# Performance work log

Hardware: AMD Instinct MI355X
Metric: run time of the kernel (lower is better)

The kernel has to match this reference:

```python
import jax, jax.numpy as jnp
import numpy as np

N_NODES = 50000
N_EDGES = 600000
D = 128
NUM_GRAPHS = 64


def gcn_conv(x, W, b, edge_index, edge_weight, n):
    """PyG GCNConv: y = D^-1/2 (A+I) D^-1/2 (x W) + b, with self-loop weight 1."""
    h = x @ W  # [n, out]
    src, dst = edge_index[0], edge_index[1]
    if edge_weight is None:
        edge_weight = jnp.ones(src.shape, dtype=x.dtype)
    # append self loops
    loop = jnp.arange(n)
    src_f = jnp.concatenate([src, loop])
    dst_f = jnp.concatenate([dst, loop])
    w_f = jnp.concatenate([edge_weight, jnp.ones((n,), dtype=x.dtype)])
    deg = jax.ops.segment_sum(w_f, dst_f, num_segments=n)
    dis = jnp.where(deg > 0, jax.lax.rsqrt(jnp.maximum(deg, 1e-12)), 0.0)
    norm = dis[src_f] * w_f * dis[dst_f]  # [E+n]
    msg = h[src_f] * norm[:, None]
    out = jax.ops.segment_sum(msg, dst_f, num_segments=n)
    return out + b


def setup_inputs() -> dict:
    key = jax.random.key(0)
    ks = jax.random.split(key, 24)
    def w(k, shape, scale=0.05):
        return jax.random.normal(k, shape, dtype=jnp.float32) * scale
    inp = {
        'x': jax.random.normal(ks[0], (N_NODES, D), dtype=jnp.float32),
        'edge_index': jax.random.randint(ks[1], (2, N_EDGES), 0, N_NODES),
        'edge_attr': jax.random.uniform(ks[2], (N_EDGES, 4), dtype=jnp.float32),
        'batch': jnp.sort(jax.random.randint(ks[3], (N_NODES,), 0, NUM_GRAPHS)),
        'W1A': w(ks[4], (D, D)), 'b1A': jnp.zeros((D,), jnp.float32),
        'W1B': w(ks[5], (D, D)), 'b1B': jnp.zeros((D,), jnp.float32),
        'W1C': w(ks[6], (D, D)), 'b1C': jnp.zeros((D,), jnp.float32),
        'W1D': w(ks[7], (D, D)), 'b1D': jnp.zeros((D,), jnp.float32),
        'W2': w(ks[8], (4 * D, 2 * D)), 'b2': jnp.zeros((2 * D,), jnp.float32),
        'W3': w(ks[9], (2 * D, D)), 'b3': jnp.zeros((D,), jnp.float32),
        'Wm1': w(ks[10], (2 * D, 8)), 'bm1': jnp.zeros((8,), jnp.float32),
        'Wm2': w(ks[11], (8, 2)), 'bm2': jnp.zeros((2,), jnp.float32),
    }
    return inp


def reference(x, edge_index, edge_attr, batch, W1A, b1A, W1B, b1B, W1C, b1C,
              W1D, b1D, W2, b2, W3, b3, Wm1, bm1, Wm2, bm2):
    n = x.shape[0]
    xA = jax.nn.relu(gcn_conv(x, W1A, b1A, edge_index, edge_attr[:, 0], n))
    xB = jax.nn.relu(gcn_conv(x, W1B, b1B, edge_index, edge_attr[:, 1], n))
    xC = jax.nn.relu(gcn_conv(x, W1C, b1C, edge_index, edge_attr[:, 2], n))
    xD = jax.nn.relu(gcn_conv(x, W1D, b1D, edge_index, edge_attr[:, 3], n))
    h = jnp.concatenate([xA, xB, xC, xD], axis=1)  # [n, 4D]
    h = jax.nn.relu(gcn_conv(h, W2, b2, edge_index, None, n))
    h = gcn_conv(h, W3, b3, edge_index, None, n)  # [n, D]
    # global mean / max pool over graphs
    counts = jax.ops.segment_sum(jnp.ones((n,), h.dtype), batch, num_segments=NUM_GRAPHS)
    sums = jax.ops.segment_sum(h, batch, num_segments=NUM_GRAPHS)
    mean = sums / jnp.maximum(counts, 1.0)[:, None]
    mx = jax.ops.segment_max(h, batch, num_segments=NUM_GRAPHS)
    mx = jnp.where(counts[:, None] > 0, mx, 0.0)
    g = jnp.concatenate([mean, mx], axis=1)  # [G, 2D]
    # dropout is identity in eval mode
    logits = jax.nn.relu(g @ Wm1 + bm1) @ Wm2 + bm2
    return logits
```

## Files before the change

kernel.cpp:

```cpp
#include <hip/hip_runtime.h>

#define DEV_INLINE __device__ __forceinline__

typedef __attribute__((ext_vector_type(8))) short bf16x8;
typedef __attribute__((ext_vector_type(4))) float floatx4;

DEV_INLINE unsigned fencode(float f) {
  unsigned u = __float_as_uint(f);
  return (u & 0x80000000u) ? ~u : (u | 0x80000000u);
}
DEV_INLINE float fdecode(unsigned k) {
  return __uint_as_float((k & 0x80000000u) ? (k ^ 0x80000000u) : ~k);
}

DEV_INLINE unsigned short bf16_rne(float x) {
  unsigned u = __float_as_uint(x);
  unsigned r = (u + 0x7FFFu + ((u >> 16) & 1u)) >> 16;
  return (unsigned short)r;
}
DEV_INLINE float bf2f(unsigned short u) {
  return __uint_as_float(((unsigned)u) << 16);
}

#pragma clang diagnostic ignored "-Waddress-space-conversion"
DEV_INLINE void gload_lds16(const void* g, void* l) {
  __builtin_amdgcn_global_load_lds(
      (const __attribute__((address_space(1))) unsigned int*)g,
      (__attribute__((address_space(3))) unsigned int*)l, 16, 0, 0);
}

__global__ __launch_bounds__(256)
void prep_kernel(const float* __restrict__ WA, const float* __restrict__ WB,
                 const float* __restrict__ WC, const float* __restrict__ WD,
                 const float* __restrict__ bA, const float* __restrict__ bB,
                 const float* __restrict__ bC, const float* __restrict__ bD,
                 const float* __restrict__ W2, const float* __restrict__ W3,
                 unsigned short* __restrict__ W1t, unsigned short* __restrict__ W2t,
                 unsigned short* __restrict__ W3t, float* __restrict__ biascat) {
  int i = blockIdx.x * 256 + threadIdx.x;
  if (i < 65536) {
    int z = i >> 14, rem = i & 16383, j = rem >> 7, k = rem & 127;
    const float* W = (z == 0) ? WA : (z == 1) ? WB : (z == 2) ? WC : WD;
    W1t[i] = bf16_rne(W[k * 128 + j]);
  } else if (i < 196608) {
    int i2 = i - 65536, j = i2 >> 9, k = i2 & 511;
    W2t[i2] = bf16_rne(W2[k * 256 + j]);
  } else if (i < 229376) {
    int i3 = i - 196608, j = i3 >> 8, k = i3 & 255;
    W3t[i3] = bf16_rne(W3[k * 128 + j]);
  } else if (i < 229888) {
    int i4 = i - 229376, c = i4 >> 7, j = i4 & 127;
    const float* b = (c == 0) ? bA : (c == 1) ? bB : (c == 2) ? bC : bD;
    biascat[i4] = b[j];
  }
}

__global__ __launch_bounds__(256)
void xcast_kernel(const float* __restrict__ x, unsigned short* __restrict__ xb, int total4) {
  int i = blockIdx.x * 256 + threadIdx.x;
  if (i >= total4) return;
  float4 v = ((const float4*)x)[i];
  ushort4 o;
  o.x = bf16_rne(v.x); o.y = bf16_rne(v.y); o.z = bf16_rne(v.z); o.w = bf16_rne(v.w);
  ((ushort4*)xb)[i] = o;
}

__global__ __launch_bounds__(256)
void hist_kernel(const int* __restrict__ ei, int* __restrict__ cnt, int E) {
  int e = blockIdx.x * 256 + threadIdx.x;
  if (e < E) atomicAdd(&cnt[ei[E + e]], 1);
}

__global__ __launch_bounds__(256)
void scan1_kernel(const int* __restrict__ cnt, int* __restrict__ local,
                  int* __restrict__ bsum, int n) {
  __shared__ int s[256];
  int tid = threadIdx.x;
  int i = blockIdx.x * 256 + tid;
  int v = (i < n) ? cnt[i] : 0;
  s[tid] = v;
  __syncthreads();
#pragma unroll
  for (int off = 1; off < 256; off <<= 1) {
    int t = (tid >= off) ? s[tid - off] : 0;
    __syncthreads();
    s[tid] += t;
    __syncthreads();
  }
  if (i < n) local[i] = s[tid] - v;
  if (tid == 255) bsum[blockIdx.x] = s[255];
}

__global__ __launch_bounds__(256)
void scan2_kernel(int* __restrict__ bsum, int nb) {
  __shared__ int s[256];
  int tid = threadIdx.x;
  int v = (tid < nb) ? bsum[tid] : 0;
  s[tid] = v;
  __syncthreads();
#pragma unroll
  for (int off = 1; off < 256; off <<= 1) {
    int t = (tid >= off) ? s[tid - off] : 0;
    __syncthreads();
    s[tid] += t;
    __syncthreads();
  }
  if (tid < nb) bsum[tid] = s[tid] - v;
}

__global__ __launch_bounds__(256)
void scan3_kernel(const int* __restrict__ local, const int* __restrict__ bsum,
                  int* __restrict__ rowptr, int* __restrict__ rowwork, int n, int E) {
  int i = blockIdx.x * 256 + threadIdx.x;
  if (i < n) {
    int rp = local[i] + bsum[blockIdx.x];
    rowptr[i] = rp;
    rowwork[i] = rp;
  }
  if (i == 0) rowptr[n] = E;
}

__global__ __launch_bounds__(256)
void fill_kernel(const int* __restrict__ ei, int* __restrict__ rowwork,
                 int* __restrict__ csr, int* __restrict__ csr_src,
                 int* __restrict__ csr_dst, int E) {
  int e = blockIdx.x * 256 + threadIdx.x;
  if (e >= E) return;
  int d = ei[E + e];
  int pos = atomicAdd(&rowwork[d], 1);
  csr[pos] = e;
  csr_src[pos] = ei[e];
  csr_dst[pos] = d;
}

__global__ __launch_bounds__(256)
void degcsr_kernel(const int* __restrict__ rowptr, const int* __restrict__ csr,
                   const float* __restrict__ eattr, float* __restrict__ dis, int n) {
  int d = blockIdx.x * 256 + threadIdx.x;
  if (d >= n) return;
  int beg = rowptr[d], end = rowptr[d + 1];
  float s0 = 1.f, s1 = 1.f, s2 = 1.f, s3 = 1.f;
  for (int i = beg; i < end; ++i) {
    int e = csr[i];
    float4 w = ((const float4*)eattr)[e];
    s0 += w.x; s1 += w.y; s2 += w.z; s3 += w.w;
  }
  dis[d]         = 1.0f / sqrtf(s0);
  dis[n + d]     = 1.0f / sqrtf(s1);
  dis[2 * n + d] = 1.0f / sqrtf(s2);
  dis[3 * n + d] = 1.0f / sqrtf(s3);
  dis[4 * n + d] = 1.0f / sqrtf(1.0f + (float)(end - beg));
}

__global__ __launch_bounds__(256)
void edgeprep_kernel(const int* __restrict__ csr, const int* __restrict__ csr_src,
                     const int* __restrict__ csr_dst, const float* __restrict__ eattr,
                     const float* __restrict__ dis, float4* __restrict__ norm4,
                     float* __restrict__ norm1, int n, int E) {
  int i = blockIdx.x * 256 + threadIdx.x;
  if (i >= E) return;
  int e = csr[i], s = csr_src[i], d = csr_dst[i];
  float4 w = ((const float4*)eattr)[e];
  float4 o;
  o.x = dis[s] * w.x * dis[d];
  o.y = dis[n + s] * w.y * dis[n + d];
  o.z = dis[2 * n + s] * w.z * dis[2 * n + d];
  o.w = dis[3 * n + s] * w.w * dis[3 * n + d];
  norm4[i] = o;
  norm1[i] = dis[4 * n + s] * dis[4 * n + d];
}

__global__ __launch_bounds__(256)
void agg4x_kernel(const unsigned short* __restrict__ xb,
                  unsigned short* __restrict__ xa,
                  const int* __restrict__ rowptr, const int* __restrict__ csr_src,
                  const float4* __restrict__ norm4, const float* __restrict__ dis,
                  int n, int npad) {
  int d = blockIdx.x * 4 + (threadIdx.x >> 6);
  if (d >= n) return;
  int t = threadIdx.x & 63;
  float dc0 = dis[d], dc1 = dis[n + d], dc2 = dis[2 * n + d], dc3 = dis[3 * n + d];
  const ushort2* x2 = (const ushort2*)xb;
  ushort2 xu = x2[(size_t)d * 64 + t];
  float xvx = bf2f(xu.x), xvy = bf2f(xu.y);
  float a0x = xvx * dc0 * dc0, a0y = xvy * dc0 * dc0;
  float a1x = xvx * dc1 * dc1, a1y = xvy * dc1 * dc1;
  float a2x = xvx * dc2 * dc2, a2y = xvy * dc2 * dc2;
  float a3x = xvx * dc3 * dc3, a3y = xvy * dc3 * dc3;
  int beg = rowptr[d], end = rowptr[d + 1];
  int i = beg;
  for (; i + 4 <= end; i += 4) {
    int s0 = csr_src[i], s1 = csr_src[i + 1], s2 = csr_src[i + 2], s3 = csr_src[i + 3];
    float4 m0 = norm4[i], m1 = norm4[i + 1], m2 = norm4[i + 2], m3 = norm4[i + 3];
    ushort2 u0 = x2[(size_t)s0 * 64 + t];
    ushort2 u1 = x2[(size_t)s1 * 64 + t];
    ushort2 u2 = x2[(size_t)s2 * 64 + t];
    ushort2 u3 = x2[(size_t)s3 * 64 + t];
    float h0x = bf2f(u0.x), h0y = bf2f(u0.y);
    float h1x = bf2f(u1.x), h1y = bf2f(u1.y);
    float h2x = bf2f(u2.x), h2y = bf2f(u2.y);
    float h3x = bf2f(u3.x), h3y = bf2f(u3.y);
    a0x += h0x * m0.x; a0y += h0y * m0.x;
    a1x += h0x * m0.y; a1y += h0y * m0.y;
    a2x += h0x * m0.z; a2y += h0y * m0.z;
    a3x += h0x * m0.w; a3y += h0y * m0.w;
    a0x += h1x * m1.x; a0y += h1y * m1.x;
    a1x += h1x * m1.y; a1y += h1y * m1.y;
    a2x += h1x * m1.z; a2y += h1y * m1.z;
    a3x += h1x * m1.w; a3y += h1y * m1.w;
    a0x += h2x * m2.x; a0y += h2y * m2.x;
    a1x += h2x * m2.y; a1y += h2y * m2.y;
    a2x += h2x * m2.z; a2y += h2y * m2.z;
    a3x += h2x * m2.w; a3y += h2y * m2.w;
    a0x += h3x * m3.x; a0y += h3y * m3.x;
    a1x += h3x * m3.y; a1y += h3y * m3.y;
    a2x += h3x * m3.z; a2y += h3y * m3.z;
    a3x += h3x * m3.w; a3y += h3y * m3.w;
  }
  for (; i < end; ++i) {
    int s = csr_src[i];
    float4 m = norm4[i];
    ushort2 u = x2[(size_t)s * 64 + t];
    float hx = bf2f(u.x), hy = bf2f(u.y);
    a0x += hx * m.x; a0y += hy * m.x;
    a1x += hx * m.y; a1y += hy * m.y;
    a2x += hx * m.z; a2y += hy * m.z;
    a3x += hx * m.w; a3y += hy * m.w;
  }
  size_t plane = (size_t)npad * 128;
  size_t base = (size_t)d * 128 + 2 * t;
  float vx[4] = {a0x, a1x, a2x, a3x};
  float vy[4] = {a0y, a1y, a2y, a3y};
#pragma unroll
  for (int z = 0; z < 4; ++z) {
    ushort2 ov; ov.x = bf16_rne(vx[z]); ov.y = bf16_rne(vy[z]);
    *(ushort2*)&xa[plane * z + base] = ov;
  }
}

template <int MODE>
DEV_INLINE void gemm_mfma_body(const unsigned short* __restrict__ A, int K,
                               const unsigned short* __restrict__ B,
                               int ldc, int col0, unsigned short* __restrict__ Cb,
                               const float* __restrict__ bias, int M, int row0) {
  __shared__ __align__(16) unsigned short As[2][128 * 32];
  __shared__ __align__(16) unsigned short Bs[2][128 * 32];
  int tid = threadIdx.x;
  int w = tid >> 6, lane = tid & 63;
  int quad = lane >> 4, lrow = lane & 15;
  int wm = (w >> 1) * 64, wn = (w & 1) * 64;

  floatx4 acc[4][4];
#pragma unroll
  for (int i = 0; i < 4; ++i)
#pragma unroll
    for (int j = 0; j < 4; ++j) acc[i][j] = {0.f, 0.f, 0.f, 0.f};

  auto stage = [&](int b, int k0) {
#pragma unroll
    for (int half = 0; half < 2; ++half) {
      int row = half * 64 + lane;
      int lb = (w * 128 + half * 64) * 8;
      gload_lds16(A + (size_t)(row0 + row) * K + k0 + w * 8, &As[b][lb]);
      gload_lds16(B + (size_t)row * K + k0 + w * 8, &Bs[b][lb]);
    }
  };

  int nk = K >> 5;
  stage(0, 0);
  int buf = 0;
  for (int kt = 0; kt < nk; ++kt) {
    __syncthreads();
    if (kt + 1 < nk) stage(buf ^ 1, (kt + 1) * 32);
    bf16x8 a_[4], b_[4];
#pragma unroll
    for (int i = 0; i < 4; ++i)
      a_[i] = *(const bf16x8*)&As[buf][(quad * 128 + wm + i * 16 + lrow) * 8];
#pragma unroll
    for (int j = 0; j < 4; ++j)
      b_[j] = *(const bf16x8*)&Bs[buf][(quad * 128 + wn + j * 16 + lrow) * 8];
#pragma unroll
    for (int j = 0; j < 4; ++j)
#pragma unroll
      for (int i = 0; i < 4; ++i)
        acc[i][j] = __builtin_amdgcn_mfma_f32_16x16x32_bf16(a_[i], b_[j], acc[i][j], 0, 0, 0);
    buf ^= 1;
  }
#pragma unroll
  for (int i = 0; i < 4; ++i) {
#pragma unroll
    for (int j = 0; j < 4; ++j) {
      int colL = wn + j * 16 + lrow;
#pragma unroll
      for (int r = 0; r < 4; ++r) {
        int row = row0 + wm + i * 16 + quad * 4 + r;
        if (row < M) {
          float v = acc[i][j][r];
          if (MODE == 1) v = fmaxf(v + bias[colL], 0.0f);
          Cb[(size_t)row * ldc + col0 + colL] = bf16_rne(v);
        }
      }
    }
  }
}

__global__ __launch_bounds__(256)
void gemm_l1_mfma(const unsigned short* __restrict__ xa,
                  const unsigned short* __restrict__ W1t,
                  const float* __restrict__ biascat,
                  unsigned short* __restrict__ h1, int M, int npad) {
  int z = blockIdx.z;
  gemm_mfma_body<1>(xa + (size_t)z * npad * 128, 128, W1t + z * 16384,
                    512, z * 128, h1, biascat + z * 128, M, blockIdx.x * 128);
}

__global__ __launch_bounds__(256)
void gemm_bf16out(const unsigned short* __restrict__ A, int K,
                  const unsigned short* __restrict__ B,
                  unsigned short* __restrict__ Cb, int ldc, int M) {
  gemm_mfma_body<2>(A, K, B + (size_t)blockIdx.y * 128 * K, ldc,
                    blockIdx.y * 128, Cb, nullptr, M, blockIdx.x * 128);
}

template <int VEC, bool RELU, int OMODE>
__global__ __launch_bounds__(256)
void agg1_kernel(const unsigned short* __restrict__ hb, float* __restrict__ out,
                 unsigned short* __restrict__ ob,
                 const int* __restrict__ rowptr, const int* __restrict__ csr_src,
                 const float* __restrict__ norm1, const float* __restrict__ dis1,
                 const float* __restrict__ bias, int n) {
  constexpr int DOUT = VEC * 64;
  int d = blockIdx.x * 4 + (threadIdx.x >> 6);
  if (d >= n) return;
  int t = threadIdx.x & 63;
  float dd = dis1[d];
  float acc[VEC];
  {
    float sw = dd * dd;
#pragma unroll
    for (int k = 0; k < VEC; ++k) acc[k] = bf2f(hb[(size_t)d * DOUT + t * VEC + k]) * sw;
  }
  int beg = rowptr[d], end = rowptr[d + 1];
  int i = beg;
  for (; i + 4 <= end; i += 4) {
    int s0 = csr_src[i], s1 = csr_src[i + 1], s2 = csr_src[i + 2], s3 = csr_src[i + 3];
    float m0 = norm1[i], m1 = norm1[i + 1], m2 = norm1[i + 2], m3 = norm1[i + 3];
    if (VEC == 4) {
      ushort4 u0 = *(const ushort4*)&hb[(size_t)s0 * DOUT + t * 4];
      ushort4 u1 = *(const ushort4*)&hb[(size_t)s1 * DOUT + t * 4];
      ushort4 u2 = *(const ushort4*)&hb[(size_t)s2 * DOUT + t * 4];
      ushort4 u3 = *(const ushort4*)&hb[(size_t)s3 * DOUT + t * 4];
      acc[0] += bf2f(u0.x) * m0; acc[1] += bf2f(u0.y) * m0;
      acc[2 % VEC] += bf2f(u0.z) * m0; acc[3 % VEC] += bf2f(u0.w) * m0;
      acc[0] += bf2f(u1.x) * m1; acc[1] += bf2f(u1.y) * m1;
      acc[2 % VEC] += bf2f(u1.z) * m1; acc[3 % VEC] += bf2f(u1.w) * m1;
      acc[0] += bf2f(u2.x) * m2; acc[1] += bf2f(u2.y) * m2;
      acc[2 % VEC] += bf2f(u2.z) * m2; acc[3 % VEC] += bf2f(u2.w) * m2;
      acc[0] += bf2f(u3.x) * m3; acc[1] += bf2f(u3.y) * m3;
      acc[2 % VEC] += bf2f(u3.z) * m3; acc[3 % VEC] += bf2f(u3.w) * m3;
    } else {
      ushort2 u0 = *(const ushort2*)&hb[(size_t)s0 * DOUT + t * 2];
      ushort2 u1 = *(const ushort2*)&hb[(size_t)s1 * DOUT + t * 2];
      ushort2 u2 = *(const ushort2*)&hb[(size_t)s2 * DOUT + t * 2];
      ushort2 u3 = *(const ushort2*)&hb[(size_t)s3 * DOUT + t * 2];
      acc[0] += bf2f(u0.x) * m0; acc[1 % VEC] += bf2f(u0.y) * m0;
      acc[0] += bf2f(u1.x) * m1; acc[1 % VEC] += bf2f(u1.y) * m1;
      acc[0] += bf2f(u2.x) * m2; acc[1 % VEC] += bf2f(u2.y) * m2;
      acc[0] += bf2f(u3.x) * m3; acc[1 % VEC] += bf2f(u3.y) * m3;
    }
  }
  for (; i < end; ++i) {
    int s = csr_src[i];
    float nrm = norm1[i];
    if (VEC == 4) {
      ushort4 u = *(const ushort4*)&hb[(size_t)s * DOUT + t * 4];
      acc[0] += bf2f(u.x) * nrm; acc[1] += bf2f(u.y) * nrm;
      acc[2 % VEC] += bf2f(u.z) * nrm; acc[3 % VEC] += bf2f(u.w) * nrm;
    } else {
      ushort2 u = *(const ushort2*)&hb[(size_t)s * DOUT + t * 2];
      acc[0] += bf2f(u.x) * nrm; acc[1 % VEC] += bf2f(u.y) * nrm;
    }
  }
#pragma unroll
  for (int k = 0; k < VEC; ++k) {
    float r = acc[k] + bias[t * VEC + k];
    if (RELU) r = fmaxf(r, 0.0f);
    if (OMODE == 1) {
      ob[(size_t)d * DOUT + t * VEC + k] = bf16_rne(r);
    } else {
      out[(size_t)d * DOUT + t * VEC + k] = r;
    }
  }
}

__global__ __launch_bounds__(128)
void pool_kernel(const float* __restrict__ h3, const int* __restrict__ batch,
                 float* __restrict__ gsum, unsigned* __restrict__ gmax, int n) {
  int c = threadIdx.x;
  int start = blockIdx.x * 32;
  int end = min(start + 32, n);
  int curg = -1;
  float s = 0.0f, m = -3.402823466e38f;
  for (int i = start; i < end; ++i) {
    int g = batch[i];
    if (g != curg) {
      if (curg >= 0) {
        atomicAdd(&gsum[curg * 128 + c], s);
        atomicMax(&gmax[curg * 128 + c], fencode(m));
      }
      curg = g; s = 0.0f; m = -3.402823466e38f;
    }
    float v = h3[(size_t)i * 128 + c];
    s += v;
    m = fmaxf(m, v);
  }
  if (curg >= 0) {
    atomicAdd(&gsum[curg * 128 + c], s);
    atomicMax(&gmax[curg * 128 + c], fencode(m));
  }
}

__global__ __launch_bounds__(512)
void mlp_kernel(const float* __restrict__ gsum, const unsigned* __restrict__ gmax,
                const int* __restrict__ batch, int n, const float* __restrict__ Wm1,
                const float* __restrict__ bm1, const float* __restrict__ Wm2,
                const float* __restrict__ bm2, float* __restrict__ out) {
  __shared__ float hid[64][8];
  int t = threadIdx.x;
  int gi = t >> 3, u = t & 7;
  auto lb = [&](int key) {
    int lo = 0, hi = n;
    while (lo < hi) {
      int mid = (lo + hi) >> 1;
      if (batch[mid] < key) lo = mid + 1; else hi = mid;
    }
    return lo;
  };
  int cnt = lb(gi + 1) - lb(gi);
  float inv = 1.0f / fmaxf((float)cnt, 1.0f);
  float s = bm1[u];
  for (int k = 0; k < 128; ++k) {
    float mean = gsum[gi * 128 + k] * inv;
    s += mean * Wm1[k * 8 + u];
  }
  for (int k = 0; k < 128; ++k) {
    float mx = (cnt > 0) ? fdecode(gmax[gi * 128 + k]) : 0.0f;
    s += mx * Wm1[(128 + k) * 8 + u];
  }
  hid[gi][u] = fmaxf(s, 0.0f);
  __syncthreads();
  if (t < 128) {
    int g2 = t >> 1, o = t & 1;
    float s2 = bm2[o];
#pragma unroll
    for (int uu = 0; uu < 8; ++uu) s2 += hid[g2][uu] * Wm2[uu * 2 + o];
    out[g2 * 2 + o] = s2;
  }
}

extern "C" void kernel_launch(void* const* d_in, const int* in_sizes, int n_in,
                              void* d_out, int out_size, void* d_ws, size_t ws_size,
                              hipStream_t stream) {
  const float* x     = (const float*)d_in[0];
  const int*   ei    = (const int*)d_in[1];
  const float* eattr = (const float*)d_in[2];
  const int*   batch = (const int*)d_in[3];
  const float* W1A = (const float*)d_in[4],  *b1A = (const float*)d_in[5];
  const float* W1B = (const float*)d_in[6],  *b1B = (const float*)d_in[7];
  const float* W1C = (const float*)d_in[8],  *b1C = (const float*)d_in[9];
  const float* W1D = (const float*)d_in[10], *b1D = (const float*)d_in[11];
  const float* W2  = (const float*)d_in[12], *b2  = (const float*)d_in[13];
  const float* W3  = (const float*)d_in[14], *b3  = (const float*)d_in[15];
  const float* Wm1 = (const float*)d_in[16], *bm1 = (const float*)d_in[17];
  const float* Wm2 = (const float*)d_in[18], *bm2 = (const float*)d_in[19];
  float* out = (float*)d_out;

  const int n = in_sizes[0] / 128;
  const int E = in_sizes[1] / 2;
  const int npad = (n + 127) & ~127;
  const int nmb = npad / 128;

  char* ws = (char*)d_ws;
  size_t off = 0;
  auto alloc = [&](size_t bytes) -> void* {
    void* p = ws + off;
    off += (bytes + 255) & ~(size_t)255;
    return p;
  };

  float*    dis     = (float*)alloc((size_t)5 * n * 4);
  int*      rowptr  = (int*)alloc(((size_t)n + 1) * 4);
  int*      rowwork = (int*)alloc((size_t)n * 4);
  int*      local   = (int*)alloc((size_t)n * 4);
  int*      bsum    = (int*)alloc(256 * 4);
  size_t zoff = off;
  int*      cnt     = (int*)alloc((size_t)n * 4);
  float*    gsum    = (float*)alloc(64 * 128 * 4);
  unsigned* gmax    = (unsigned*)alloc(64 * 128 * 4);
  size_t zbytes = off - zoff;
  int*      csr     = (int*)alloc((size_t)E * 4);
  int*      csr_src = (int*)alloc((size_t)E * 4);
  int*      csr_dst = (int*)alloc((size_t)E * 4);
  float4*   norm4   = (float4*)alloc((size_t)E * 16);
  float*    norm1   = (float*)alloc((size_t)E * 4);
  unsigned short* W1t = (unsigned short*)alloc(65536 * 2);
  unsigned short* W2t = (unsigned short*)alloc(131072 * 2);
  unsigned short* W3t = (unsigned short*)alloc(32768 * 2);
  float*    biascat = (float*)alloc(512 * 4);
  unsigned short* xb   = (unsigned short*)alloc((size_t)npad * 128 * 2);
  unsigned short* bufA = (unsigned short*)alloc((size_t)npad * 512 * 2);
  unsigned short* bufB = (unsigned short*)alloc((size_t)npad * 512 * 2);
  alloc(4096);

  unsigned short* xa      = bufA;
  unsigned short* h1      = bufB;
  unsigned short* h2pre_b = bufA;
  unsigned short* h2      = bufB;
  unsigned short* h3pre_b = bufA;
  float*          h3      = (float*)(bufB + (size_t)npad * 256);

  hipMemsetAsync(ws + zoff, 0, zbytes, stream);

  prep_kernel<<<(229888 + 255) / 256, 256, 0, stream>>>(
      W1A, W1B, W1C, W1D, b1A, b1B, b1C, b1D, W2, W3,
      W1t, W2t, W3t, biascat);
  xcast_kernel<<<((n * 32) + 255) / 256, 256, 0, stream>>>(x, xb, n * 32);

  int nb = (n + 255) / 256;
  hist_kernel<<<(E + 255) / 256, 256, 0, stream>>>(ei, cnt, E);
  scan1_kernel<<<nb, 256, 0, stream>>>(cnt, local, bsum, n);
  scan2_kernel<<<1, 256, 0, stream>>>(bsum, nb);
  scan3_kernel<<<nb, 256, 0, stream>>>(local, bsum, rowptr, rowwork, n, E);
  fill_kernel<<<(E + 255) / 256, 256, 0, stream>>>(ei, rowwork, csr, csr_src, csr_dst, E);
  degcsr_kernel<<<(n + 255) / 256, 256, 0, stream>>>(rowptr, csr, eattr, dis, n);
  edgeprep_kernel<<<(E + 255) / 256, 256, 0, stream>>>(csr, csr_src, csr_dst, eattr,
                                                       dis, norm4, norm1, n, E);

  int nodeblk = (n + 3) / 4;
  agg4x_kernel<<<nodeblk, 256, 0, stream>>>(xb, xa, rowptr, csr_src, norm4, dis, n, npad);
  gemm_l1_mfma<<<dim3(nmb, 1, 4), 256, 0, stream>>>(xa, W1t, biascat, h1, n, npad);
  gemm_bf16out<<<dim3(nmb, 2), 256, 0, stream>>>(h1, 512, W2t, h2pre_b, 256, n);
  agg1_kernel<4, true, 1><<<nodeblk, 256, 0, stream>>>(h2pre_b, nullptr, h2,
                                                       rowptr, csr_src, norm1,
                                                       dis + (size_t)4 * n, b2, n);
  gemm_bf16out<<<dim3(nmb, 1), 256, 0, stream>>>(h2, 256, W3t, h3pre_b, 128, n);
  agg1_kernel<2, false, 0><<<nodeblk, 256, 0, stream>>>(h3pre_b, h3, nullptr,
                                                        rowptr, csr_src, norm1,
                                                        dis + (size_t)4 * n, b3, n);

  pool_kernel<<<(n + 31) / 32, 128, 0, stream>>>(h3, batch, gsum, gmax, n);
  mlp_kernel<<<1, 512, 0, stream>>>(gsum, gmax, batch, n, Wm1, bm1, Wm2, bm2, out);
}
```

Measured before the change: 496.8 us.

## Fuse x cast into prep, store edge weights in CSR order, widen layer-2 GEMM

Merges the x-to-bf16 cast into the weight-prep kernel to save a launch. The fill kernel now writes edge attributes in CSR order, so the degree and edge-prep kernels read them sequentially instead of gathering through an edge-id indirection. The layer-2 GEMM becomes a single 512-thread kernel whose blocks each compute a 128x256 output tile, so A is loaded once instead of twice, at the cost of more LDS and register use per block.

```diff
diff --git a/kernel.cpp b/kernel.cpp
--- a/kernel.cpp
+++ b/kernel.cpp
@@ -36,7 +36,9 @@
                  const float* __restrict__ bC, const float* __restrict__ bD,
                  const float* __restrict__ W2, const float* __restrict__ W3,
                  unsigned short* __restrict__ W1t, unsigned short* __restrict__ W2t,
-                 unsigned short* __restrict__ W3t, float* __restrict__ biascat) {
+                 unsigned short* __restrict__ W3t, float* __restrict__ biascat,
+                 const float* __restrict__ x, unsigned short* __restrict__ xb,
+                 int total4) {
   int i = blockIdx.x * 256 + threadIdx.x;
   if (i < 65536) {
     int z = i >> 14, rem = i & 16383, j = rem >> 7, k = rem & 127;
@@ -53,16 +55,12 @@
     const float* b = (c == 0) ? bA : (c == 1) ? bB : (c == 2) ? bC : bD;
     biascat[i4] = b[j];
   }
-}
-
-__global__ __launch_bounds__(256)
-void xcast_kernel(const float* __restrict__ x, unsigned short* __restrict__ xb, int total4) {
-  int i = blockIdx.x * 256 + threadIdx.x;
-  if (i >= total4) return;
-  float4 v = ((const float4*)x)[i];
-  ushort4 o;
-  o.x = bf16_rne(v.x); o.y = bf16_rne(v.y); o.z = bf16_rne(v.z); o.w = bf16_rne(v.w);
-  ((ushort4*)xb)[i] = o;
+  if (i < total4) {
+    float4 v = ((const float4*)x)[i];
+    ushort4 o;
+    o.x = bf16_rne(v.x); o.y = bf16_rne(v.y); o.z = bf16_rne(v.z); o.w = bf16_rne(v.w);
+    ((ushort4*)xb)[i] = o;
+  }
 }
 
 __global__ __launch_bounds__(256)
@@ -121,28 +119,27 @@
 }
 
 __global__ __launch_bounds__(256)
-void fill_kernel(const int* __restrict__ ei, int* __restrict__ rowwork,
-                 int* __restrict__ csr, int* __restrict__ csr_src,
-                 int* __restrict__ csr_dst, int E) {
+void fill_kernel(const int* __restrict__ ei, const float* __restrict__ eattr,
+                 int* __restrict__ rowwork, int* __restrict__ csr_src,
+                 int* __restrict__ csr_dst, float4* __restrict__ csr_w, int E) {
   int e = blockIdx.x * 256 + threadIdx.x;
   if (e >= E) return;
   int d = ei[E + e];
   int pos = atomicAdd(&rowwork[d], 1);
-  csr[pos] = e;
   csr_src[pos] = ei[e];
   csr_dst[pos] = d;
-}
-
-__global__ __launch_bounds__(256)
-void degcsr_kernel(const int* __restrict__ rowptr, const int* __restrict__ csr,
-                   const float* __restrict__ eattr, float* __restrict__ dis, int n) {
+  csr_w[pos] = ((const float4*)eattr)[e];
+}
+
+__global__ __launch_bounds__(256)
+void degcsr_kernel(const int* __restrict__ rowptr, const float4* __restrict__ csr_w,
+                   float* __restrict__ dis, int n) {
   int d = blockIdx.x * 256 + threadIdx.x;
   if (d >= n) return;
   int beg = rowptr[d], end = rowptr[d + 1];
   float s0 = 1.f, s1 = 1.f, s2 = 1.f, s3 = 1.f;
   for (int i = beg; i < end; ++i) {
-    int e = csr[i];
-    float4 w = ((const float4*)eattr)[e];
+    float4 w = csr_w[i];
     s0 += w.x; s1 += w.y; s2 += w.z; s3 += w.w;
   }
   dis[d]         = 1.0f / sqrtf(s0);
@@ -153,14 +150,14 @@
 }
 
 __global__ __launch_bounds__(256)
-void edgeprep_kernel(const int* __restrict__ csr, const int* __restrict__ csr_src,
-                     const int* __restrict__ csr_dst, const float* __restrict__ eattr,
-                     const float* __restrict__ dis, float4* __restrict__ norm4,
-                     float* __restrict__ norm1, int n, int E) {
+void edgeprep_kernel(const int* __restrict__ csr_src, const int* __restrict__ csr_dst,
+                     const float4* __restrict__ csr_w, const float* __restrict__ dis,
+                     float4* __restrict__ norm4, float* __restrict__ norm1,
+                     int n, int E) {
   int i = blockIdx.x * 256 + threadIdx.x;
   if (i >= E) return;
-  int e = csr[i], s = csr_src[i], d = csr_dst[i];
-  float4 w = ((const float4*)eattr)[e];
+  int s = csr_src[i], d = csr_dst[i];
+  float4 w = csr_w[i];
   float4 o;
   o.x = dis[s] * w.x * dis[d];
   o.y = dis[n + s] * w.y * dis[n + d];
@@ -322,6 +319,71 @@
                     blockIdx.y * 128, Cb, nullptr, M, blockIdx.x * 128);
 }
 
+__global__ __launch_bounds__(512)
+void gemm_l2_wide(const unsigned short* __restrict__ A,
+                  const unsigned short* __restrict__ B,
+                  unsigned short* __restrict__ Cb, int M) {
+  constexpr int K = 512;
+  __shared__ __align__(16) unsigned short As[2][128 * 32];
+  __shared__ __align__(16) unsigned short Bs[2][256 * 32];
+  int tid = threadIdx.x;
+  int w = tid >> 6, lane = tid & 63;
+  int quad = lane >> 4, lrow = lane & 15;
+  int wm = (w >> 2) * 64, wn = (w & 3) * 64;
+  int row0 = blockIdx.x * 128;
+  int u0 = w * 64;
+
+  floatx4 acc[4][4];
+#pragma unroll
+  for (int i = 0; i < 4; ++i)
+#pragma unroll
+    for (int j = 0; j < 4; ++j) acc[i][j] = {0.f, 0.f, 0.f, 0.f};
+
+  auto stage = [&](int b, int k0) {
+    gload_lds16(A + (size_t)(row0 + (tid & 127)) * K + k0 + (tid >> 7) * 8,
+                &As[b][u0 * 8]);
+#pragma unroll
+    for (int inst = 0; inst < 2; ++inst) {
+      int u = inst * 512 + tid;
+      gload_lds16(B + (size_t)(u & 255) * K + k0 + (u >> 8) * 8,
+                  &Bs[b][(inst * 512 + u0) * 8]);
+    }
+  };
+
+  stage(0, 0);
+  int buf = 0;
+#pragma unroll 1
+  for (int kt = 0; kt < 16; ++kt) {
+    __syncthreads();
+    if (kt + 1 < 16) stage(buf ^ 1, (kt + 1) * 32);
+    bf16x8 a_[4], b_[4];
+#pragma unroll
+    for (int i = 0; i < 4; ++i)
+      a_[i] = *(const bf16x8*)&As[buf][(quad * 128 + wm + i * 16 + lrow) * 8];
+#pragma unroll
+    for (int j = 0; j < 4; ++j)
+      b_[j] = *(const bf16x8*)&Bs[buf][(quad * 256 + wn + j * 16 + lrow) * 8];
+#pragma unroll
+    for (int j = 0; j < 4; ++j)
+#pragma unroll
+      for (int i = 0; i < 4; ++i)
+        acc[i][j] = __builtin_amdgcn_mfma_f32_16x16x32_bf16(a_[i], b_[j], acc[i][j], 0, 0, 0);
+    buf ^= 1;
+  }
+#pragma unroll
+  for (int i = 0; i < 4; ++i) {
+#pragma unroll
+    for (int j = 0; j < 4; ++j) {
+      int colL = wn + j * 16 + lrow;
+#pragma unroll
+      for (int r = 0; r < 4; ++r) {
+        int row = row0 + wm + i * 16 + quad * 4 + r;
+        if (row < M) Cb[(size_t)row * 256 + colL] = bf16_rne(acc[i][j][r]);
+      }
+    }
+  }
+}
+
 template <int VEC, bool RELU, int OMODE>
 __global__ __launch_bounds__(256)
 void agg1_kernel(const unsigned short* __restrict__ hb, float* __restrict__ out,
@@ -498,9 +560,9 @@
   float*    gsum    = (float*)alloc(64 * 128 * 4);
   unsigned* gmax    = (unsigned*)alloc(64 * 128 * 4);
   size_t zbytes = off - zoff;
-  int*      csr     = (int*)alloc((size_t)E * 4);
   int*      csr_src = (int*)alloc((size_t)E * 4);
   int*      csr_dst = (int*)alloc((size_t)E * 4);
+  float4*   csr_w   = (float4*)alloc((size_t)E * 16);
   float4*   norm4   = (float4*)alloc((size_t)E * 16);
   float*    norm1   = (float*)alloc((size_t)E * 4);
   unsigned short* W1t = (unsigned short*)alloc(65536 * 2);
@@ -521,25 +583,25 @@
 
   hipMemsetAsync(ws + zoff, 0, zbytes, stream);
 
-  prep_kernel<<<(229888 + 255) / 256, 256, 0, stream>>>(
+  int total4 = n * 32;
+  prep_kernel<<<(total4 + 255) / 256, 256, 0, stream>>>(
       W1A, W1B, W1C, W1D, b1A, b1B, b1C, b1D, W2, W3,
-      W1t, W2t, W3t, biascat);
-  xcast_kernel<<<((n * 32) + 255) / 256, 256, 0, stream>>>(x, xb, n * 32);
+      W1t, W2t, W3t, biascat, x, xb, total4);
 
   int nb = (n + 255) / 256;
   hist_kernel<<<(E + 255) / 256, 256, 0, stream>>>(ei, cnt, E);
   scan1_kernel<<<nb, 256, 0, stream>>>(cnt, local, bsum, n);
   scan2_kernel<<<1, 256, 0, stream>>>(bsum, nb);
   scan3_kernel<<<nb, 256, 0, stream>>>(local, bsum, rowptr, rowwork, n, E);
-  fill_kernel<<<(E + 255) / 256, 256, 0, stream>>>(ei, rowwork, csr, csr_src, csr_dst, E);
-  degcsr_kernel<<<(n + 255) / 256, 256, 0, stream>>>(rowptr, csr, eattr, dis, n);
-  edgeprep_kernel<<<(E + 255) / 256, 256, 0, stream>>>(csr, csr_src, csr_dst, eattr,
+  fill_kernel<<<(E + 255) / 256, 256, 0, stream>>>(ei, eattr, rowwork, csr_src, csr_dst, csr_w, E);
+  degcsr_kernel<<<(n + 255) / 256, 256, 0, stream>>>(rowptr, csr_w, dis, n);
+  edgeprep_kernel<<<(E + 255) / 256, 256, 0, stream>>>(csr_src, csr_dst, csr_w,
                                                        dis, norm4, norm1, n, E);
 
   int nodeblk = (n + 3) / 4;
   agg4x_kernel<<<nodeblk, 256, 0, stream>>>(xb, xa, rowptr, csr_src, norm4, dis, n, npad);
   gemm_l1_mfma<<<dim3(nmb, 1, 4), 256, 0, stream>>>(xa, W1t, biascat, h1, n, npad);
-  gemm_bf16out<<<dim3(nmb, 2), 256, 0, stream>>>(h1, 512, W2t, h2pre_b, 256, n);
+  gemm_l2_wide<<<nmb, 512, 0, stream>>>(h1, W2t, h2pre_b, n);
   agg1_kernel<4, true, 1><<<nodeblk, 256, 0, stream>>>(h2pre_b, nullptr, h2,
                                                        rowptr, csr_src, norm1,
                                                        dis + (size_t)4 * n, b2, n);
```

Measured after the change: 477.3 us. 1.04x faster.
